# Kernel optimization log

Measured on AMD Instinct MI355X. Metric: run time of the kernel, lower is better.

Reference implementation:

```python
import jax, jax.numpy as jnp
import numpy as np

N = 100000       # nodes
E = 1600000      # edges
NFEAT = 128
NHID = 128
NCLASS = 64
NHEAD = 4
NLAYER = 3
LRELU_ALPHA = 0.2


def setup_inputs() -> dict:
    key = jax.random.key(0)
    ks = jax.random.split(key, 7)
    x = jax.random.normal(ks[0], (N, NFEAT), jnp.float32)
    edge_index = jax.random.randint(ks[1], (2, E), 0, N, jnp.int32)
    # xavier-uniform-ish init scales (gain for relu baked into scale roughly)
    Win = jax.random.normal(ks[2], (NFEAT, NHID), jnp.float32) * (2.0 / (NFEAT + NHID)) ** 0.5
    b_in = jnp.zeros((NHID,), jnp.float32)
    # per hidden layer, per head: a split into (src, dst) halves of the (1, 2*in) vector
    a_hid = jax.random.normal(ks[3], (NLAYER - 1, NHEAD, 2, NHID), jnp.float32) * 0.1
    W_hid = jax.random.normal(ks[4], (NLAYER - 1, NHEAD, NHID, NHID // NHEAD), jnp.float32) * (2.0 / (NHID + NHID // NHEAD)) ** 0.5
    a_out = jax.random.normal(ks[5], (2, NHID), jnp.float32) * 0.1
    W_out = jax.random.normal(ks[6], (NHID, NCLASS), jnp.float32) * (2.0 / (NHID + NCLASS)) ** 0.5
    return dict(x=x, edge_index=edge_index, Win=Win, b_in=b_in,
                a_hid=a_hid, W_hid=W_hid, a_out=a_out, W_out=W_out)


def _segment_softmax(logits, seg, n):
    # numerically stable softmax over groups defined by seg (axis 0)
    m = jax.ops.segment_max(logits, seg, num_segments=n)
    e = jnp.exp(logits - m[seg])
    s = jax.ops.segment_sum(e, seg, num_segments=n)
    return e / s[seg]


def _gat_conv(h, row, col, a, W):
    # h: [N, D]; a: [H, 2, D]; W: [H, D, Dh]
    n = h.shape[0]
    H = a.shape[0]
    s_src = h @ a[:, 0, :].T  # [N, H]
    s_dst = h @ a[:, 1, :].T  # [N, H]
    logits = jax.nn.leaky_relu(s_src[row] + s_dst[col], LRELU_ALPHA)  # [E, H]
    alpha = _segment_softmax(logits, row, n)  # softmax grouped by row (edge_index[0])
    h_col = h[col]  # [E, D] gathered once, reused per head
    outs = []
    for hd in range(H):  # small fixed head loop keeps peak memory at [E, D]
        agg = jax.ops.segment_sum(alpha[:, hd, None] * h_col, row, num_segments=n)  # [N, D]
        outs.append(agg @ W[hd])  # weight applied AFTER aggregation, as in source
    return jnp.concatenate(outs, axis=1)


def reference(x, edge_index, Win, b_in, a_hid, W_hid, a_out, W_out):
    row, col = edge_index[0], edge_index[1]
    h = jax.nn.elu(x @ Win + b_in)  # in_linear + ELU (dropout is identity in eval/p=0)
    for l in range(a_hid.shape[0]):
        h = jax.nn.elu(_gat_conv(h, row, col, a_hid[l], W_hid[l]))
    # final conv: single head to nclass, no activation
    return _gat_conv(h, row, col, a_out[None], W_out[None])
```

## Files before the change

kernel.cpp:

```cpp
#include <hip/hip_runtime.h>
#include <hip/hip_bf16.h>
#include <cstdint>
#include <cstddef>

#define LRELU_ALPHA 0.2f
#define LOG2E 1.44269504088896f

typedef __attribute__((ext_vector_type(8))) short short8;
typedef __attribute__((ext_vector_type(4))) float f32x4;
typedef _Float16 h2v __attribute__((ext_vector_type(2)));

__device__ __forceinline__ unsigned short f2bf(float f) {
    unsigned int u = __float_as_uint(f);
    unsigned int r = (u + 0x7fffu + ((u >> 16) & 1u)) >> 16;
    return (unsigned short)r;
}
__device__ __forceinline__ float bf2f(unsigned int lo16) {
    return __uint_as_float(lo16 << 16);
}
__device__ __forceinline__ unsigned int pk2(float a, float b) {
    return (unsigned int)f2bf(a) | ((unsigned int)f2bf(b) << 16);
}
__device__ __forceinline__ float fexp2(float x) {
#if __has_builtin(__builtin_amdgcn_exp2f)
    return __builtin_amdgcn_exp2f(x);
#else
    return __expf(x * 0.69314718056f);
#endif
}
__device__ __forceinline__ h2v pkrtz(float a, float b) {
#if __has_builtin(__builtin_amdgcn_cvt_pkrtz)
    auto r = __builtin_amdgcn_cvt_pkrtz(a, b);
    union { decltype(r) i; h2v o; } u;
    u.i = r;
    return u.o;
#else
    h2v r; r.x = (_Float16)a; r.y = (_Float16)b; return r;
#endif
}
__device__ __forceinline__ unsigned int pack_lo(unsigned int a, unsigned int b) {
#if __has_builtin(__builtin_amdgcn_perm)
    return __builtin_amdgcn_perm(a, b, 0x01000504u);
#else
    return (a & 0xffffu) | (b << 16);
#endif
}
__device__ __forceinline__ unsigned int pack_hi(unsigned int a, unsigned int b) {
#if __has_builtin(__builtin_amdgcn_perm)
    return __builtin_amdgcn_perm(a, b, 0x03020706u);
#else
    return (a >> 16) | (b & 0xffff0000u);
#endif
}
union U32H2 { unsigned int u; h2v h; };
__device__ __forceinline__ float dot2f(unsigned int a, h2v w, float acc) {
    U32H2 c; c.u = a;
#if __has_builtin(__builtin_amdgcn_fdot2)
    return __builtin_amdgcn_fdot2(c.h, w, acc, false);
#else
    return acc + (float)c.h.x * (float)w.x + (float)c.h.y * (float)w.y;
#endif
}


__global__ void hist_repack_k(const int* __restrict__ ei, int* __restrict__ counts8,
                              int* __restrict__ rank,
                              float* __restrict__ sdA, float* __restrict__ sdB,
                              float* __restrict__ sdC, unsigned int* __restrict__ hW,
                              const float* __restrict__ Win, const float* __restrict__ Whid,
                              const float* __restrict__ ahid, const float* __restrict__ Wout,
                              const float* __restrict__ aout,
                              unsigned short* __restrict__ W0, unsigned short* __restrict__ W1,
                              unsigned short* __restrict__ W2, unsigned short* __restrict__ W3,
                              int N_, int E_, int EB8) {
    int bid = blockIdx.x;
    if (bid < EB8) {
        int rep = bid & 7;
        int base = (bid * 256 + threadIdx.x) * 8;
        int* cnt = counts8 + (size_t)rep * N_;
        if (base + 8 <= E_) {
            int4 a = *(const int4*)&ei[base];
            int4 b = *(const int4*)&ei[base + 4];
            int rk[8];
            rk[0] = atomicAdd(&cnt[a.x], 1);
            rk[1] = atomicAdd(&cnt[a.y], 1);
            rk[2] = atomicAdd(&cnt[a.z], 1);
            rk[3] = atomicAdd(&cnt[a.w], 1);
            rk[4] = atomicAdd(&cnt[b.x], 1);
            rk[5] = atomicAdd(&cnt[b.y], 1);
            rk[6] = atomicAdd(&cnt[b.z], 1);
            rk[7] = atomicAdd(&cnt[b.w], 1);
            *(int4*)&rank[base]     = make_int4(rk[0], rk[1], rk[2], rk[3]);
            *(int4*)&rank[base + 4] = make_int4(rk[4], rk[5], rk[6], rk[7]);
        } else if (base < E_) {
            for (int j = 0; j < 8 && base + j < E_; j++)
                rank[base + j] = atomicAdd(&cnt[ei[base + j]], 1);
        }
        if (bid == 0) {
            int t = threadIdx.x;
            if (t < 4) { sdA[N_ * 4 + t] = -1e30f; sdB[N_ * 4 + t] = -1e30f; }
            if (t == 4) sdC[N_] = -1e30f;
            if (t >= 32 && t < 64)  hW[(size_t)N_ * 32 + (t - 32)] = 0u;
            if (t >= 64 && t < 128) hW[(size_t)N_ * 64 + (t - 64)] = 0u;
        }
    } else {
        int i = (bid - EB8) * 256 + threadIdx.x;
        if (i < 16384) {
            int n = i >> 7, k = i & 127;
            W0[i] = f2bf(Win[k * 128 + n]);
        } else if (i < 16384 + 2 * 18432) {
            int j = i - 16384;
            int l = j / 18432;
            int jj = j - l * 18432;
            int n = jj >> 7, k = jj & 127;
            float v;
            if (n < 128) {
                int hd = n >> 5, c = n & 31;
                v = Whid[(size_t)l * 16384 + (hd * 128 + k) * 32 + c];
            } else if (n < 136) {
                int ch = n - 128;
                v = ahid[((size_t)l * 8 + ch) * 128 + k] * LOG2E;
            } else {
                v = 0.f;
            }
            (l ? W2 : W1)[jj] = f2bf(v);
        } else if (i < 16384 + 2 * 18432 + 10240) {
            int j = i - (16384 + 2 * 18432);
            int n = j >> 7, k = j & 127;
            float v;
            if (n < 64)       v = Wout[k * 64 + n];
            else if (n < 66)  v = aout[(n - 64) * 128 + k] * LOG2E;
            else              v = 0.f;
            W3[j] = f2bf(v);
        }
    }
}

__global__ void scan_sums_k(int* bsum, int nb) {
    __shared__ int s[512];
    int v = ((int)threadIdx.x < nb) ? bsum[threadIdx.x] : 0;
    s[threadIdx.x] = v;
    __syncthreads();
    for (int d = 1; d < 512; d <<= 1) {
        int t_ = ((int)threadIdx.x >= d) ? s[threadIdx.x - d] : 0;
        __syncthreads();
        s[threadIdx.x] += t_;
        __syncthreads();
    }
    if ((int)threadIdx.x < nb) bsum[threadIdx.x] = s[threadIdx.x] - v;
}

__global__ void finalize_k(const int* __restrict__ tmp, const int* __restrict__ bsum,
                           const int* __restrict__ counts8, int* __restrict__ base8,
                           int* __restrict__ off, int* __restrict__ scol, int N_, int n) {
    int i = blockIdx.x * 256 + threadIdx.x;
    if (i < n) {
        int end = tmp[i] + bsum[blockIdx.x];
        off[i + 1] = end;
        int c[8], cnt = 0;
        #pragma unroll
        for (int r = 0; r < 8; r++) { c[r] = counts8[(size_t)r * n + i]; cnt += c[r]; }
        int padded = (cnt + 7) & ~7;
        int pos = end - padded;
        #pragma unroll
        for (int r = 0; r < 8; r++) { base8[(size_t)r * n + i] = pos; pos += c[r]; }
        for (; pos < end; pos++) scol[pos] = N_;
    }
    if (i == 0) off[0] = 0;
}

__global__ void scatter8_k(const int* __restrict__ ei, const int* __restrict__ rank,
                           const int* __restrict__ base8, int* __restrict__ scol,
                           int N_, int E_) {
    int rep = blockIdx.x & 7;
    int base = (blockIdx.x * 256 + threadIdx.x) * 8;
    const int* cb = base8 + (size_t)rep * N_;
    if (base + 8 <= E_) {
        int4 a   = *(const int4*)&ei[base];
        int4 b   = *(const int4*)&ei[base + 4];
        int4 ra  = *(const int4*)&rank[base];
        int4 rb  = *(const int4*)&rank[base + 4];
        int4 ca  = *(const int4*)&ei[E_ + base];
        int4 cb4 = *(const int4*)&ei[E_ + base + 4];
        scol[cb[a.x] + ra.x] = ca.x;
        scol[cb[a.y] + ra.y] = ca.y;
        scol[cb[a.z] + ra.z] = ca.z;
        scol[cb[a.w] + ra.w] = ca.w;
        scol[cb[b.x] + rb.x] = cb4.x;
        scol[cb[b.y] + rb.y] = cb4.y;
        scol[cb[b.z] + rb.z] = cb4.z;
        scol[cb[b.w] + rb.w] = cb4.w;
    } else if (base < E_) {
        for (int j = 0; j < 8 && base + j < E_; j++) {
            int r = ei[base + j];
            scol[cb[r] + rank[base + j]] = ei[E_ + base + j];
        }
    }
}


template <int KJ, int KJA, bool ELU_ACT, bool BIAS, int OUTM, bool ABF16, int SC_H>
__device__ __forceinline__ void gemm_body(const void* __restrict__ Xv,
                                          const unsigned short* __restrict__ WT,
                                          const float* __restrict__ bias,
                                          void* __restrict__ Yv,
                                          float* __restrict__ ssn,
                                          float* __restrict__ sdn, int nRows,
                                          int bid, unsigned short* sWT) {
    constexpr int NT = KJA / 16;
    constexpr int NTS = KJ / 16;
    constexpr int WS = 136;
    int t = threadIdx.x;
    for (int i = t; i < KJA * 16; i += 256) {
        int n = i >> 4, k8 = i & 15;
        uint4 v = *(const uint4*)&WT[n * 128 + k8 * 8];
        *(uint4*)&sWT[n * WS + k8 * 8] = v;
    }
    __syncthreads();

    int lane = t & 63;
    int wv = t >> 6;
    int m0 = bid * 128 + wv * 32;
    int l16 = lane & 15;
    int q4 = lane >> 4;

    short8 afr[4][2];
    #pragma unroll
    for (int rt = 0; rt < 2; rt++) {
        int row = m0 + rt * 16 + l16;
        bool vr = row < nRows;
        if (ABF16) {
            const unsigned int* xp = (const unsigned int*)Xv + (size_t)row * 64 + q4 * 4;
            #pragma unroll
            for (int kk = 0; kk < 4; kk++) {
                uint4 u = make_uint4(0u, 0u, 0u, 0u);
                if (vr) u = *(const uint4*)(xp + kk * 16);
                afr[kk][rt] = *(short8*)&u;
            }
        } else {
            const float* xp = (const float*)Xv + (size_t)row * 128 + q4 * 8;
            #pragma unroll
            for (int kk = 0; kk < 4; kk++) {
                float4 a0 = make_float4(0.f, 0.f, 0.f, 0.f), a1 = a0;
                if (vr) {
                    a0 = *(const float4*)(xp + kk * 32);
                    a1 = *(const float4*)(xp + kk * 32 + 4);
                }
                unsigned int u[4];
                u[0] = pk2(a0.x, a0.y); u[1] = pk2(a0.z, a0.w);
                u[2] = pk2(a1.x, a1.y); u[3] = pk2(a1.z, a1.w);
                afr[kk][rt] = *(short8*)u;
            }
        }
    }

    f32x4 acc[2][NT] = {};
    #pragma unroll
    for (int kk = 0; kk < 4; kk++) {
        #pragma unroll
        for (int ct = 0; ct < NT; ct++) {
            int n = ct * 16 + l16;
            short8 bf = *(const short8*)&sWT[n * WS + kk * 32 + q4 * 8];
            #pragma unroll
            for (int rt = 0; rt < 2; rt++)
                acc[rt][ct] = __builtin_amdgcn_mfma_f32_16x16x32_bf16(afr[kk][rt], bf, acc[rt][ct], 0, 0, 0);
        }
    }

    #pragma unroll
    for (int rt = 0; rt < 2; rt++) {
        #pragma unroll
        for (int q = 0; q < 4; q++) {
            int row = m0 + rt * 16 + q4 * 4 + q;
            if (row >= nRows) continue;
            #pragma unroll
            for (int ct = 0; ct < NTS; ct++) {
                int colc = ct * 16 + l16;
                float v = acc[rt][ct][q];
                if (BIAS) v += bias[colc];
                if (ELU_ACT) v = v > 0.f ? v : (__expf(v) - 1.f);
                if (OUTM == 1) {
                    ((unsigned short*)Yv)[(size_t)row * KJ + colc] = f2bf(v);
                } else if (OUTM == 2) {
                    union { _Float16 hf; unsigned short us; } cv;
                    cv.hf = (_Float16)v;
                    ((unsigned short*)Yv)[(size_t)row * KJ + colc] = cv.us;
                } else {
                    ((float*)Yv)[(size_t)row * KJ + colc] = v;
                }
            }
            if (SC_H > 0) {
                if (l16 < 2 * SC_H) {
                    float v = acc[rt][NT - 1][q];
                    float* dst = (l16 & 1) ? sdn : ssn;
                    dst[row * SC_H + (l16 >> 1)] = v;
                }
            }
        }
    }
}

template <int KJ, int KJA, bool ELU_ACT, bool BIAS, int OUTM, bool ABF16, int SC_H>
__global__ __launch_bounds__(256) void gemm_mfma(const void* __restrict__ Xv,
                                                 const unsigned short* __restrict__ WT,
                                                 const float* __restrict__ bias,
                                                 void* __restrict__ Yv,
                                                 float* __restrict__ ssn,
                                                 float* __restrict__ sdn, int nRows) {
    __shared__ unsigned short sWT[KJA * 136];
    gemm_body<KJ, KJA, ELU_ACT, BIAS, OUTM, ABF16, SC_H>(
        Xv, WT, bias, Yv, ssn, sdn, nRows, blockIdx.x, sWT);
}

__global__ __launch_bounds__(256) void gemm0_scan_k(const float* __restrict__ x,
                                                    const unsigned short* __restrict__ WT0,
                                                    const float* __restrict__ bin,
                                                    unsigned int* __restrict__ hb,
                                                    const int* __restrict__ counts8,
                                                    int* __restrict__ tmp,
                                                    int* __restrict__ bsum,
                                                    int nRows, int n, int RT) {
    __shared__ unsigned short sWT[128 * 136];
    int bid = blockIdx.x;
    if (bid < RT) {
        gemm_body<128, 128, true, true, 1, false, 0>(
            x, WT0, bin, hb, nullptr, nullptr, nRows, bid, sWT);
    } else {
        int* s = (int*)sWT;
        int sb = bid - RT;
        int i = sb * 256 + threadIdx.x;
        int v = 0;
        if (i < n) {
            int c = 0;
            #pragma unroll
            for (int r = 0; r < 8; r++) c += counts8[(size_t)r * n + i];
            v = (c + 7) & ~7;
        }
        s[threadIdx.x] = v;
        __syncthreads();
        for (int d = 1; d < 256; d <<= 1) {
            int t_ = (threadIdx.x >= (unsigned)d) ? s[threadIdx.x - d] : 0;
            __syncthreads();
            s[threadIdx.x] += t_;
            __syncthreads();
        }
        if (i < n) tmp[i] = s[threadIdx.x];
        if (threadIdx.x == 255) bsum[sb] = s[255];
    }
}


template <int DHT, int H, bool ELU_ACT, bool BF16O>
__global__ __launch_bounds__(256) void edge_agg_v(const unsigned int* __restrict__ hW2,
                                                  const float* __restrict__ ssrc,
                                                  const float* __restrict__ sdst,
                                                  const int* __restrict__ off,
                                                  const int* __restrict__ scol,
                                                  void* __restrict__ outv, int nRows) {
    constexpr int FPL = DHT / 16;
    constexpr int UPL = FPL / 2;
    int lane = threadIdx.x & 63;
    int sub = lane & 15;
    int g = lane >> 4;
    int wv = threadIdx.x >> 6;
    int r = __builtin_amdgcn_readfirstlane(blockIdx.x * 4 + wv);
    if (r >= nRows) return;
    int begin = off[r], end = off[r + 1];

    int head = (H == 4) ? (sub >> 2) : 0;
    float ssl = ssrc[r * H + head];

    float acc[FPL] = {};
    float den = 0.f;

    for (int i = begin; i < end; i += 8) {
        int2 cc = *(const int2*)&scol[i + 2 * g];
        int cA = cc.x, cB = cc.y;
        float sdA = sdst[cA * H + head];
        float sdB = sdst[cB * H + head];
        unsigned int hA[UPL], hB[UPL];
        int oA = cA * (DHT / 2) + sub * UPL;
        int oB = cB * (DHT / 2) + sub * UPL;
        if (UPL == 4) {
            *(uint4*)hA = *(const uint4*)&hW2[oA];
            *(uint4*)hB = *(const uint4*)&hW2[oB];
        } else {
            *(uint2*)hA = *(const uint2*)&hW2[oA];
            *(uint2*)hB = *(const uint2*)&hW2[oB];
        }
        float lgA = ssl + sdA;
        float wA = fexp2(fmaxf(lgA, LRELU_ALPHA * lgA));
        float lgB = ssl + sdB;
        float wB = fexp2(fmaxf(lgB, LRELU_ALPHA * lgB));
        den += wA + wB;
        h2v w2 = pkrtz(wA, wB);
        #pragma unroll
        for (int q = 0; q < UPL; q++) {
            acc[2 * q]     = dot2f(pack_lo(hA[q], hB[q]), w2, acc[2 * q]);
            acc[2 * q + 1] = dot2f(pack_hi(hA[q], hB[q]), w2, acc[2 * q + 1]);
        }
    }

    #pragma unroll
    for (int s = 16; s < 64; s <<= 1) {
        den += __shfl_xor(den, s);
        #pragma unroll
        for (int p = 0; p < FPL; p++) acc[p] += __shfl_xor(acc[p], s);
    }
    float inv = den > 0.f ? 1.f / den : 0.f;

    float v[FPL];
    #pragma unroll
    for (int p = 0; p < FPL; p++) {
        float tv = acc[p] * inv;
        if (ELU_ACT) tv = tv > 0.f ? tv : (__expf(tv) - 1.f);
        v[p] = tv;
    }

    if (DHT == 128) {
        if (BF16O)
            ((unsigned int*)outv)[(size_t)r * 64 + sub * 4 + g] = pk2(v[2 * g], v[2 * g + 1]);
        else
            *(float2*)&((float*)outv)[(size_t)r * 128 + sub * 8 + 2 * g] =
                make_float2(v[2 * g], v[2 * g + 1]);
    } else {
        ((float*)outv)[(size_t)r * DHT + sub * FPL + g] = v[g];
    }
}


extern "C" void kernel_launch(void* const* d_in, const int* in_sizes, int n_in,
                              void* d_out, int out_size, void* d_ws, size_t ws_size,
                              hipStream_t stream) {
    const float* x    = (const float*)d_in[0];
    const int*   ei   = (const int*)d_in[1];
    const float* Win  = (const float*)d_in[2];
    const float* bin  = (const float*)d_in[3];
    const float* ahid = (const float*)d_in[4];
    const float* Whid = (const float*)d_in[5];
    const float* aout = (const float*)d_in[6];
    const float* Wout = (const float*)d_in[7];
    float* out = (float*)d_out;

    const int N_ = in_sizes[0] / 128;
    const int E_ = in_sizes[1] / 2;

    char* p = (char*)d_ws;
    auto alloc = [&](size_t bytes) {
        char* q = p;
        p += (bytes + 511) & ~(size_t)511;
        return q;
    };
    int* counts8 = (int*)alloc((size_t)N_ * 8 * 4);
    int* base8   = (int*)alloc((size_t)N_ * 8 * 4);
    int* rank    = (int*)alloc((size_t)(E_ + 8) * 4);
    int* tmp     = (int*)alloc((size_t)N_ * 4);
    int* off     = (int*)alloc((size_t)(N_ + 1) * 4);
    int* bsum    = (int*)alloc(4096);
    int* scol    = (int*)alloc((size_t)(E_ + 8 * N_ + 64) * 4);
    float* ssrcA = (float*)alloc((size_t)(N_ + 1) * 4 * 4);
    float* sdstA = (float*)alloc((size_t)(N_ + 1) * 4 * 4);
    float* ssrcB = (float*)alloc((size_t)(N_ + 1) * 4 * 4);
    float* sdstB = (float*)alloc((size_t)(N_ + 1) * 4 * 4);
    float* ssrcC = (float*)alloc((size_t)(N_ + 1) * 4);
    float* sdstC = (float*)alloc((size_t)(N_ + 1) * 4);
    unsigned int* hb  = (unsigned int*)alloc((size_t)N_ * 64 * 4);
    unsigned int* hWb = (unsigned int*)alloc((size_t)(N_ + 1) * 64 * 4);
    unsigned short* WT0 = (unsigned short*)alloc(128 * 128 * 2);
    unsigned short* WT1 = (unsigned short*)alloc(144 * 128 * 2);
    unsigned short* WT2 = (unsigned short*)alloc(144 * 128 * 2);
    unsigned short* WT3 = (unsigned short*)alloc(80 * 128 * 2);

    int NB  = (N_ + 255) / 256;
    int EB8 = (E_ + 2047) / 2048;
    int RT  = (N_ + 127) / 128;
    int NW  = (N_ + 3) / 4;

    (void)hipMemsetAsync(counts8, 0, (size_t)N_ * 8 * 4, stream);
    hist_repack_k<<<EB8 + 248, 256, 0, stream>>>(
        ei, counts8, rank, sdstA, sdstB, sdstC, hWb,
        Win, Whid, ahid, Wout, aout, WT0, WT1, WT2, WT3, N_, E_, EB8);
    gemm0_scan_k<<<RT + NB, 256, 0, stream>>>(
        x, WT0, bin, hb, counts8, tmp, bsum, N_, N_, RT);
    scan_sums_k<<<1, 512, 0, stream>>>(bsum, NB);
    finalize_k<<<NB, 256, 0, stream>>>(tmp, bsum, counts8, base8, off, scol, N_, N_);
    scatter8_k<<<EB8, 256, 0, stream>>>(ei, rank, base8, scol, N_, E_);

    gemm_mfma<128, 144, false, false, 2, true, 4><<<RT, 256, 0, stream>>>(
        hb, WT1, nullptr, hWb, ssrcA, sdstA, N_);
    edge_agg_v<128, 4, true, true><<<NW, 256, 0, stream>>>(
        hWb, ssrcA, sdstA, off, scol, hb, N_);

    gemm_mfma<128, 144, false, false, 2, true, 4><<<RT, 256, 0, stream>>>(
        hb, WT2, nullptr, hWb, ssrcB, sdstB, N_);
    edge_agg_v<128, 4, true, true><<<NW, 256, 0, stream>>>(
        hWb, ssrcB, sdstB, off, scol, hb, N_);

    gemm_mfma<64, 80, false, false, 2, true, 1><<<RT, 256, 0, stream>>>(
        hb, WT3, nullptr, hWb, ssrcC, sdstC, N_);
    edge_agg_v<64, 1, false, false><<<NW, 256, 0, stream>>>(
        hWb, ssrcC, sdstC, off, scol, out, N_);
}
```

Measured before the change: 456.5 us.

## Fold block-sum scan into finalize and fuse edge scatter with first hidden GEMM

```diff
diff --git a/kernel.cpp b/kernel.cpp
--- a/kernel.cpp
+++ b/kernel.cpp
@@ -136,26 +136,25 @@
     }
 }
 
-__global__ void scan_sums_k(int* bsum, int nb) {
-    __shared__ int s[512];
-    int v = ((int)threadIdx.x < nb) ? bsum[threadIdx.x] : 0;
-    s[threadIdx.x] = v;
-    __syncthreads();
-    for (int d = 1; d < 512; d <<= 1) {
-        int t_ = ((int)threadIdx.x >= d) ? s[threadIdx.x - d] : 0;
-        __syncthreads();
-        s[threadIdx.x] += t_;
-        __syncthreads();
-    }
-    if ((int)threadIdx.x < nb) bsum[threadIdx.x] = s[threadIdx.x] - v;
-}
-
 __global__ void finalize_k(const int* __restrict__ tmp, const int* __restrict__ bsum,
                            const int* __restrict__ counts8, int* __restrict__ base8,
                            int* __restrict__ off, int* __restrict__ scol, int N_, int n) {
-    int i = blockIdx.x * 256 + threadIdx.x;
+    __shared__ int sred[256];
+    int t = threadIdx.x;
+    int acc = 0;
+    for (int j = t; j < (int)blockIdx.x; j += 256) acc += bsum[j];
+    sred[t] = acc;
+    __syncthreads();
+    #pragma unroll
+    for (int d = 128; d > 0; d >>= 1) {
+        if (t < d) sred[t] += sred[t + d];
+        __syncthreads();
+    }
+    int prefix = sred[0];
+
+    int i = blockIdx.x * 256 + t;
     if (i < n) {
-        int end = tmp[i] + bsum[blockIdx.x];
+        int end = tmp[i] + prefix;
         off[i + 1] = end;
         int c[8], cnt = 0;
         #pragma unroll
@@ -167,35 +166,6 @@
         for (; pos < end; pos++) scol[pos] = N_;
     }
     if (i == 0) off[0] = 0;
-}
-
-__global__ void scatter8_k(const int* __restrict__ ei, const int* __restrict__ rank,
-                           const int* __restrict__ base8, int* __restrict__ scol,
-                           int N_, int E_) {
-    int rep = blockIdx.x & 7;
-    int base = (blockIdx.x * 256 + threadIdx.x) * 8;
-    const int* cb = base8 + (size_t)rep * N_;
-    if (base + 8 <= E_) {
-        int4 a   = *(const int4*)&ei[base];
-        int4 b   = *(const int4*)&ei[base + 4];
-        int4 ra  = *(const int4*)&rank[base];
-        int4 rb  = *(const int4*)&rank[base + 4];
-        int4 ca  = *(const int4*)&ei[E_ + base];
-        int4 cb4 = *(const int4*)&ei[E_ + base + 4];
-        scol[cb[a.x] + ra.x] = ca.x;
-        scol[cb[a.y] + ra.y] = ca.y;
-        scol[cb[a.z] + ra.z] = ca.z;
-        scol[cb[a.w] + ra.w] = ca.w;
-        scol[cb[b.x] + rb.x] = cb4.x;
-        scol[cb[b.y] + rb.y] = cb4.y;
-        scol[cb[b.z] + rb.z] = cb4.z;
-        scol[cb[b.w] + rb.w] = cb4.w;
-    } else if (base < E_) {
-        for (int j = 0; j < 8 && base + j < E_; j++) {
-            int r = ei[base + j];
-            scol[cb[r] + rank[base + j]] = ei[E_ + base + j];
-        }
-    }
 }
 
 
@@ -349,6 +319,45 @@
     }
 }
 
+__global__ __launch_bounds__(256) void scatter_gemm1_k(
+        const int* __restrict__ ei, const int* __restrict__ rank,
+        const int* __restrict__ base8, int* __restrict__ scol, int N_, int E_, int EB8,
+        const unsigned int* __restrict__ hb, const unsigned short* __restrict__ WT1,
+        unsigned int* __restrict__ hWb, float* __restrict__ ssrcA,
+        float* __restrict__ sdstA, int nRows) {
+    __shared__ unsigned short sWT[144 * 136];
+    int bid = blockIdx.x;
+    if (bid < EB8) {
+        int rep = bid & 7;
+        int base = (bid * 256 + threadIdx.x) * 8;
+        const int* cb = base8 + (size_t)rep * N_;
+        if (base + 8 <= E_) {
+            int4 a   = *(const int4*)&ei[base];
+            int4 b   = *(const int4*)&ei[base + 4];
+            int4 ra  = *(const int4*)&rank[base];
+            int4 rb  = *(const int4*)&rank[base + 4];
+            int4 ca  = *(const int4*)&ei[E_ + base];
+            int4 cb4 = *(const int4*)&ei[E_ + base + 4];
+            scol[cb[a.x] + ra.x] = ca.x;
+            scol[cb[a.y] + ra.y] = ca.y;
+            scol[cb[a.z] + ra.z] = ca.z;
+            scol[cb[a.w] + ra.w] = ca.w;
+            scol[cb[b.x] + rb.x] = cb4.x;
+            scol[cb[b.y] + rb.y] = cb4.y;
+            scol[cb[b.z] + rb.z] = cb4.z;
+            scol[cb[b.w] + rb.w] = cb4.w;
+        } else if (base < E_) {
+            for (int j = 0; j < 8 && base + j < E_; j++) {
+                int r = ei[base + j];
+                scol[cb[r] + rank[base + j]] = ei[E_ + base + j];
+            }
+        }
+    } else {
+        gemm_body<128, 144, false, false, 2, true, 4>(
+            hb, WT1, nullptr, hWb, ssrcA, sdstA, nRows, bid - EB8, sWT);
+    }
+}
+
 
 template <int DHT, int H, bool ELU_ACT, bool BF16O>
 __global__ __launch_bounds__(256) void edge_agg_v(const unsigned int* __restrict__ hW2,
@@ -482,12 +491,9 @@
         Win, Whid, ahid, Wout, aout, WT0, WT1, WT2, WT3, N_, E_, EB8);
     gemm0_scan_k<<<RT + NB, 256, 0, stream>>>(
         x, WT0, bin, hb, counts8, tmp, bsum, N_, N_, RT);
-    scan_sums_k<<<1, 512, 0, stream>>>(bsum, NB);
     finalize_k<<<NB, 256, 0, stream>>>(tmp, bsum, counts8, base8, off, scol, N_, N_);
-    scatter8_k<<<EB8, 256, 0, stream>>>(ei, rank, base8, scol, N_, E_);
-
-    gemm_mfma<128, 144, false, false, 2, true, 4><<<RT, 256, 0, stream>>>(
-        hb, WT1, nullptr, hWb, ssrcA, sdstA, N_);
+    scatter_gemm1_k<<<EB8 + RT, 256, 0, stream>>>(
+        ei, rank, base8, scol, N_, E_, EB8, hb, WT1, hWb, ssrcA, sdstA, N_);
     edge_agg_v<128, 4, true, true><<<NW, 256, 0, stream>>>(
         hWb, ssrcA, sdstA, off, scol, hb, N_);
 
```

New measurement: 442.6 us. 3.0% less time.
